# Performance work log

Measured on AMD Instinct MI355X. Metric: run time of the kernel, lower is better.

Reference implementation:

```python
import jax, jax.numpy as jnp
import numpy as np
from functools import partial

TAU = 2.0
BN_EPS = 1e-5
SG_ALPHA = 4.0  # spikingjelly surrogate.Sigmoid default

@jax.custom_vjp
def heaviside(x):
    return (x >= 0.0).astype(x.dtype)

def _heaviside_fwd(x):
    return heaviside(x), x

def _heaviside_bwd(x, g):
    s = jax.nn.sigmoid(SG_ALPHA * x)
    return (g * SG_ALPHA * s * (1.0 - s),)

heaviside.defvjp(_heaviside_fwd, _heaviside_bwd)

def lif(x_seq, v_threshold=1.0):
    # MultiStepLIFNode: tau=2, decay_input=True, v_reset=0 (hard reset), detach_reset
    def step(v, x):
        v = v + (x - v) / TAU
        s = heaviside(v - v_threshold)
        v = v * (1.0 - jax.lax.stop_gradient(s))
        return v, s
    _, s_seq = jax.lax.scan(step, jnp.zeros_like(x_seq[0]), x_seq)
    return s_seq

def conv1x1_bn(x, w, gamma, beta, mean, var, b=None):
    # x: [T,B,C,N]; w: [Cout,Cin]; 1x1 conv == channel matmul; BN in eval mode
    y = jnp.einsum('oc,tbcn->tbon', w, x)
    if b is not None:
        y = y + b[:, None]
    inv = gamma / jnp.sqrt(var + BN_EPS)
    return y * inv[:, None] + (beta - mean * inv)[:, None]

def setup_inputs() -> dict:
    key = jax.random.key(0)
    ks = jax.random.split(key, 24)
    T, B, C, N = 4, 32, 384, 196
    d = {}
    d['x'] = jax.random.normal(ks[0], (T, B, C, N), dtype=jnp.float32)
    d['policy'] = jax.random.uniform(ks[1], (T * B, N, 1), dtype=jnp.float32)
    scale = 1.0 / np.sqrt(C)
    for i, p in enumerate(['q', 'k', 'v', 'proj']):
        base = 2 + i * 5
        d[p + '_w'] = jax.random.normal(ks[base], (C, C), dtype=jnp.float32) * scale
        d[p + '_gamma'] = jnp.ones((C,), jnp.float32)
        d[p + '_beta'] = jnp.zeros((C,), jnp.float32)
        d[p + '_mean'] = jax.random.normal(ks[base + 1], (C,), dtype=jnp.float32) * 0.1
        d[p + '_var'] = jax.random.uniform(ks[base + 2], (C,), dtype=jnp.float32, minval=0.5, maxval=1.5)
    d['proj_b'] = jnp.zeros((C,), jnp.float32)
    return d

def _to_heads(s, H):
    T, B, C, N = s.shape
    # [T,B,C,N] -> [T,B,N,H,D] -> [T,B,H,N,D]
    return s.transpose(0, 1, 3, 2).reshape(T, B, N, H, C // H).transpose(0, 1, 3, 2, 4)

def reference(x, policy, q_w, q_gamma, q_beta, q_mean, q_var,
              k_w, k_gamma, k_beta, k_mean, k_var,
              v_w, v_gamma, v_beta, v_mean, v_var,
              proj_w, proj_gamma, proj_beta, proj_mean, proj_var, proj_b):
    T, B, C, N = x.shape
    H = 12
    attn_scale = 0.25
    q = _to_heads(lif(conv1x1_bn(x, q_w, q_gamma, q_beta, q_mean, q_var)), H)
    k = _to_heads(lif(conv1x1_bn(x, k_w, k_gamma, k_beta, k_mean, k_var)), H)
    v = _to_heads(lif(conv1x1_bn(x, v_w, v_gamma, v_beta, v_mean, v_var)), H)
    attn = jnp.einsum('tbhnd,tbhmd->tbhnm', q, k)
    # attention_policy: attn *= (policy + (1-policy)*eye)
    pol = policy.reshape(T, B, 1, 1, N)
    eye = jnp.eye(N, dtype=attn.dtype)
    attn = attn * (pol + (1.0 - pol) * eye)
    y = jnp.einsum('tbhnm,tbhmd->tbhnd', attn, v) * attn_scale
    y = y.transpose(0, 1, 2, 4, 3).reshape(T, B, C, N)
    y = lif(y, v_threshold=0.5)
    y = conv1x1_bn(y, proj_w, proj_gamma, proj_beta, proj_mean, proj_var, b=proj_b)
    return lif(y)
```

## Files before the change

kernel.cpp:

```cpp
#include <hip/hip_runtime.h>

typedef unsigned int u32;
typedef __bf16 bf16x8 __attribute__((ext_vector_type(8)));
typedef __bf16 bf16x4v __attribute__((ext_vector_type(4)));
typedef _Float16 f16x8 __attribute__((ext_vector_type(8)));
typedef float f32x4 __attribute__((ext_vector_type(4)));

#define Tn 4
#define Bn 32
#define Cn 384
#define Nn 196
#define Hn 12
#define CNn (Cn*Nn)
#define BCNn (Bn*CNn)
#define BHNn (Bn*Hn*Nn)
#define PBITS (Tn*BHNn)
#define TBCNn (Tn*BCNn)
#define NCOLS 6272
#define WSZ 147456

__device__ __forceinline__ void split3(float v, __bf16& h, __bf16& m, __bf16& l) {
  h = (__bf16)v;  float r = v - (float)h;
  m = (__bf16)r;  float r2 = r - (float)m;
  l = (__bf16)r2;
}
__device__ __forceinline__ void split2h(float v, _Float16& h, _Float16& l) {
  h = (_Float16)v;  l = (_Float16)(v - (float)h);
}

__device__ __forceinline__ void gl_lds16(const void* g, void* l) {
  __builtin_amdgcn_global_load_lds(
      (const __attribute__((address_space(1))) unsigned int*)g,
      (__attribute__((address_space(3))) unsigned int*)l, 16, 0, 0);
}

struct WSplitArgs {
  const float* w[4]; const float* g[4]; const float* be[4];
  const float* mu[4]; const float* va[4]; const float* bias;
};
__global__ __launch_bounds__(256) void prep(
    WSplitArgs a, _Float16* __restrict__ wsp16, __bf16* __restrict__ wspb,
    float* __restrict__ shv, const float* __restrict__ x,
    _Float16* __restrict__ xs) {
  __shared__ float tile[49 * 130];
  const int bx = blockIdx.x;
  const int tid = threadIdx.x;
  if (bx < 2304) {
    const int i = bx * 256 + tid;
    const int p = i / WSZ, r = i - p * WSZ;
    const int o = r / Cn, cc = r - o * Cn;
    const float iv = a.g[p][o] / sqrtf(a.va[p][o] + 1e-5f);
    const float wv = a.w[p][r] * iv;
    const int toff = ((o >> 4) * 12 + (cc >> 5)) * 512 +
                     (((cc >> 3) & 3) << 7) + ((o & 15) << 3) + (cc & 7);
    if (p < 3) {
      _Float16 h, l;
      split2h(wv, h, l);
      wsp16[(size_t)(p * 2 + 0) * WSZ + toff] = h;
      wsp16[(size_t)(p * 2 + 1) * WSZ + toff] = l;
    } else {
      __bf16 h, m, l;
      split3(wv, h, m, l);
      wspb[(size_t)0 * WSZ + toff] = h;
      wspb[(size_t)1 * WSZ + toff] = m;
      wspb[(size_t)2 * WSZ + toff] = l;
    }
    if (cc == 0) {
      float sh = a.be[p][o] - a.mu[p][o] * iv;
      if (p == 3) sh += a.bias[o] * iv;
      shv[p * Cn + o] = sh;
    }
    return;
  }
  const int bid2 = bx - 2304;
  const int t = bid2 & 3, b = (bid2 >> 2) & 31, zz = bid2 >> 7;
  const int ct = zz >> 2, nch = zz & 3;
  const int c0 = ct * 128, n0 = nch * 49;
  for (int idx = tid; idx < 49 * 128; idx += 256) {
    const int n = idx % 49, c = idx / 49;
    tile[n * 130 + c] = x[(size_t)t * BCNn + (size_t)b * CNn +
                          (size_t)(c0 + c) * Nn + n0 + n];
  }
  __syncthreads();
  for (int idx = tid; idx < 49 * 64; idx += 256) {
    const int cp = idx & 63, n = idx >> 6;
    const float v0 = tile[n * 130 + cp * 2];
    const float v1 = tile[n * 130 + cp * 2 + 1];
    _Float16 h0, l0, h1, l1;
    split2h(v0, h0, l0);
    split2h(v1, h1, l1);
    const size_t col = (size_t)t * NCOLS + (size_t)b * Nn + n0 + n;
    union { _Float16 f[2]; u32 u; } uh, ul;
    uh.f[0] = h0; uh.f[1] = h1;
    ul.f[0] = l0; ul.f[1] = l1;
    ((u32*)(xs + col * Cn + c0))[cp] = uh.u;
    ((u32*)(xs + (size_t)TBCNn + col * Cn + c0))[cp] = ul.u;
  }
}

__global__ __launch_bounds__(256, 2) void gemm_qkv_lif(
    const _Float16* __restrict__ xs,
    const _Float16* __restrict__ wsp16,
    const float* __restrict__ shv,
    u32* __restrict__ bq, u32* __restrict__ bk, u32* __restrict__ bv)
{
  __shared__ _Float16 Bsw[6][2][64][32];
  const int orig = blockIdx.x;
  const int xcd = orig & 7, i8 = orig >> 3;
  const int wgid = xcd * 110 + (xcd < 2 ? xcd : 2) + i8;
  const int colt = wgid / 9, v = wgid - colt * 9;
  const int col0 = colt * 64;
  const int p = v / 3, mt = v - p * 3;
  const int o0 = mt * 128;
  const int tid = threadIdx.x, lane = tid & 63, wid = tid >> 6;
  const int wm = wid >> 1, wn = wid & 1;
  const int quad = lane >> 4, nl = lane & 15;
  u32* __restrict__ bits = (p == 0) ? bq : (p == 1) ? bk : bv;

  u32 afOff[2][4];
#pragma unroll
  for (int s = 0; s < 2; ++s)
#pragma unroll
    for (int mi = 0; mi < 4; ++mi)
      afOff[s][mi] = (u32)((((p * 2 + s) * WSZ) +
                            (mt * 8 + wm * 4 + mi) * 6144) * 2) +
                     (u32)(lane * 16);
  u32 bOff[2];
#pragma unroll
  for (int i = 0; i < 2; ++i) {
    const int c = i * 256 + wid * 64 + lane;
    const int s = c >> 8, rem = c & 255, row = rem >> 2, kb = rem & 3;
    const int kbs = kb ^ ((row >> 1) & 3);
    bOff[i] = (u32)(((size_t)s * TBCNn + (size_t)(col0 + row) * Cn + kbs * 8) * 2);
  }
  const char* wB = (const char*)wsp16;
  const char* xB = (const char*)xs;
  char* bD0 = (char*)&Bsw[0][0][0][0] + wid * 1024;

#define STAGE_B(g_) do {                                                   \
    const int t_ = ((g_) / 24) * 2 + ((g_) & 1);                           \
    const int kk_ = (((g_) % 24) >> 1);                                    \
    const u32 bk_ = (u32)(kk_ * 64) + (u32)t_ * (u32)(NCOLS * Cn * 2);     \
    char* d_ = bD0 + ((g_) % 6) * 8192;                                    \
    _Pragma("unroll") for (int i_ = 0; i_ < 2; ++i_)                       \
      gl_lds16(xB + bOff[i_] + bk_, d_ + i_ * 4096);                       \
  } while (0)
#define LOAD_AF(DST, g_) do {                                              \
    const u32 ak2_ = (u32)(((g_) % 12) * 1024);                            \
    _Pragma("unroll") for (int s_ = 0; s_ < 2; ++s_)                       \
    _Pragma("unroll") for (int m_ = 0; m_ < 4; ++m_)                       \
      DST[s_][m_] = *(const f16x8*)(wB + afOff[s_][m_] + ak2_);            \
  } while (0)

  f32x4 sh_[4];
#pragma unroll
  for (int mi = 0; mi < 4; ++mi)
    sh_[mi] = *(const f32x4*)&shv[p * Cn + o0 + wm * 64 + mi * 16 + quad * 4];

  f32x4 acc0[4][2], acc1[4][2];
  f32x4 vst[4][2] = {};
  f16x8 afA[2][4], afB[2][4];

  auto epi = [&](f32x4 (&ac)[4][2], int t) {
#pragma unroll
    for (int ni = 0; ni < 2; ++ni) {
      u32 w0 = 0, w1 = 0;
#pragma unroll
      for (int mi = 0; mi < 4; ++mi) {
#pragma unroll
        for (int r = 0; r < 4; ++r) {
          const float y = ac[mi][ni][r] + sh_[mi][r];
          const float vv = vst[mi][ni][r];
          const float nv = vv + (y - vv) * 0.5f;
          const bool sk = nv >= 1.0f;
          vst[mi][ni][r] = sk ? 0.f : nv;
          const u32 b1 = sk ? 1u : 0u;
          const int pos = ((mi & 1) << 4) + (quad << 2) + r;
          if (mi < 2) w0 |= b1 << pos; else w1 |= b1 << pos;
        }
      }
      w0 |= __shfl_xor(w0, 16); w0 |= __shfl_xor(w0, 32);
      w1 |= __shfl_xor(w1, 16); w1 |= __shfl_xor(w1, 32);
      if (quad == 0) {
        const int col = col0 + wn * 32 + ni * 16 + nl;
        const int bb = col / Nn, nn = col - bb * Nn;
        u32* bp = bits + (size_t)t * BHNn +
                  ((size_t)bb * Hn + (mt * 4 + wm * 2)) * Nn + nn;
        bp[0] = w0;
        bp[Nn] = w1;
      }
    }
  };

  auto sub = [&](f16x8 (&afc)[2][4], f16x8 (&afn)[2][4], int g) {
    const int kk = g % 12;
    const int be = (2 * g) % 6, bo = (2 * g + 1) % 6;
    if (g == 23) asm volatile("s_waitcnt vmcnt(8)"  ::: "memory");
    else         asm volatile("s_waitcnt vmcnt(12)" ::: "memory");
    __builtin_amdgcn_s_barrier();
    __builtin_amdgcn_sched_barrier(0);
    if (g < 22) STAGE_B(2 * g + 4);
    if (g < 23) LOAD_AF(afn, g + 1);
    if (g < 22) STAGE_B(2 * g + 5);
    __builtin_amdgcn_sched_barrier(0);
    if (kk == 0) {
#pragma unroll
      for (int mi = 0; mi < 4; ++mi)
#pragma unroll
        for (int ni = 0; ni < 2; ++ni) {
          acc0[mi][ni] = f32x4{0.f, 0.f, 0.f, 0.f};
          acc1[mi][ni] = f32x4{0.f, 0.f, 0.f, 0.f};
        }
    }
    {
      f16x8 bfrE[2][2], bfrO[2][2];
#pragma unroll
      for (int i = 0; i < 2; ++i) {
        const int rb = wn * 32 + i * 16 + nl;
        const int kb2 = (quad ^ ((rb >> 1) & 3)) * 8;
        bfrE[0][i] = *(const f16x8*)&Bsw[be][0][rb][kb2];
        bfrE[1][i] = *(const f16x8*)&Bsw[be][1][rb][kb2];
        bfrO[0][i] = *(const f16x8*)&Bsw[bo][0][rb][kb2];
        bfrO[1][i] = *(const f16x8*)&Bsw[bo][1][rb][kb2];
      }
      __builtin_amdgcn_s_setprio(1);
#pragma unroll
      for (int mi = 0; mi < 4; ++mi)
#pragma unroll
        for (int ni = 0; ni < 2; ++ni) {
          f32x4 c = acc0[mi][ni];
          c = __builtin_amdgcn_mfma_f32_16x16x32_f16(afc[0][mi], bfrE[0][ni], c, 0, 0, 0);
          c = __builtin_amdgcn_mfma_f32_16x16x32_f16(afc[0][mi], bfrE[1][ni], c, 0, 0, 0);
          c = __builtin_amdgcn_mfma_f32_16x16x32_f16(afc[1][mi], bfrE[0][ni], c, 0, 0, 0);
          acc0[mi][ni] = c;
          f32x4 d = acc1[mi][ni];
          d = __builtin_amdgcn_mfma_f32_16x16x32_f16(afc[0][mi], bfrO[0][ni], d, 0, 0, 0);
          d = __builtin_amdgcn_mfma_f32_16x16x32_f16(afc[0][mi], bfrO[1][ni], d, 0, 0, 0);
          d = __builtin_amdgcn_mfma_f32_16x16x32_f16(afc[1][mi], bfrO[0][ni], d, 0, 0, 0);
          acc1[mi][ni] = d;
        }
      __builtin_amdgcn_s_setprio(0);
    }
    if (kk == 11) {
      const int p2 = g / 12;
      epi(acc0, p2 * 2 + 0);
      epi(acc1, p2 * 2 + 1);
    }
  };

  STAGE_B(0); STAGE_B(1); STAGE_B(2);
  LOAD_AF(afA, 0);
  STAGE_B(3);

#pragma unroll 1
  for (int gp = 0; gp < 12; ++gp) {
    sub(afA, afB, 2 * gp);
    sub(afB, afA, 2 * gp + 1);
  }
#undef STAGE_B
#undef LOAD_AF
}

#define USTR 232
#define GSTR 40
__global__ __launch_bounds__(256, 2) void attn_lif(
    const u32* __restrict__ qb, const u32* __restrict__ kb,
    const u32* __restrict__ vb, const float* __restrict__ policy,
    __bf16* __restrict__ sp) {
  __shared__ u32 qs[208], ks[224], vs_[224];
  __shared__ float ps[224];
  __shared__ __bf16 psp[3][224];
  __shared__ __bf16 Ul[3][32][USTR];
  __shared__ __bf16 GT[3][32][GSTR];
  const int bh = blockIdx.x;
  const int bN = bh / Hn;
  const int h = bh - bN * Hn;
  const int tid = threadIdx.x;
  const int lane = tid & 63, wid = tid >> 6;
  const int quad = lane >> 4, nl = lane & 15;
  const int wm1 = wid >> 1, wn1 = wid & 1;
  const __bf16 one = (__bf16)1.0f, zero = (__bf16)0.0f;

  float vst[4][2][4] = {};

  for (int t = 0; t < Tn; ++t) {
    const int tb = t * Bn + bN;
    const int gid = tb * Hn + h;
    if (t) __syncthreads();
    for (int i = tid; i < 224; i += 256) {
      const bool in = i < Nn;
      if (i < 208) qs[i] = in ? qb[(size_t)gid * Nn + i] : 0u;
      ks[i] = in ? kb[(size_t)gid * Nn + i] : 0u;
      vs_[i] = in ? vb[(size_t)gid * Nn + i] : 0u;
      const float p = in ? policy[(size_t)tb * Nn + i] : 0.f;
      ps[i] = p;
      __bf16 hh, mm, ll;
      split3(p, hh, mm, ll);
      psp[0][i] = hh; psp[1][i] = mm; psp[2][i] = ll;
    }
    __syncthreads();

#pragma unroll
    for (int it = 0; it < 7; ++it) {
      const int idx = tid + it * 256;
      const int d = idx & 31, mg = idx >> 5;
      __bf16 u4[3][4];
#pragma unroll
      for (int j = 0; j < 4; ++j) {
        const int m = mg * 4 + j;
        const bool bit = (vs_[m] >> d) & 1u;
#pragma unroll
        for (int s = 0; s < 3; ++s)
          u4[s][j] = bit ? psp[s][m] : zero;
      }
#pragma unroll
      for (int s = 0; s < 3; ++s)
        *(bf16x4v*)&Ul[s][d][mg * 4] = *(bf16x4v*)u4[s];
    }
    __syncthreads();

    f32x4 gacc = {0.f, 0.f, 0.f, 0.f};
    const int crow = wm1 * 16 + nl;
    const int drow = wn1 * 16 + nl;
#pragma unroll
    for (int slab = 0; slab < 7; ++slab) {
      const int m0 = slab * 32 + quad * 8;
      u32 kw[8];
      *(uint4*)&kw[0] = *(const uint4*)&ks[m0];
      *(uint4*)&kw[4] = *(const uint4*)&ks[m0 + 4];
      __bf16 a8[8];
#pragma unroll
      for (int j = 0; j < 8; ++j)
        a8[j] = ((kw[j] >> crow) & 1u) ? one : zero;
      const bf16x8 af = *(const bf16x8*)a8;
#pragma unroll
      for (int s = 0; s < 3; ++s)
        gacc = __builtin_amdgcn_mfma_f32_16x16x32_bf16(
            af, *(const bf16x8*)&Ul[s][drow][slab * 32 + quad * 8], gacc, 0, 0, 0);
    }
#pragma unroll
    for (int r = 0; r < 4; ++r) {
      __bf16 gh, gm, gl;
      split3(gacc[r], gh, gm, gl);
      const int cc = wm1 * 16 + quad * 4 + r;
      GT[0][drow][cc] = gh;
      GT[1][drow][cc] = gm;
      GT[2][drow][cc] = gl;
    }
    __syncthreads();

    bf16x8 bfr2[3][2];
#pragma unroll
    for (int s = 0; s < 3; ++s)
#pragma unroll
      for (int nt = 0; nt < 2; ++nt)
        bfr2[s][nt] = *(const bf16x8*)&GT[s][nt * 16 + nl][quad * 8];

    f32x4 acc2[4][2] = {};
#pragma unroll
    for (int mi = 0; mi < 4; ++mi) {
      const int lt = wid + mi * 4;
      if (lt < 13) {
        const u32 qw = qs[lt * 16 + nl];
        __bf16 a8[8];
#pragma unroll
        for (int j = 0; j < 8; ++j)
          a8[j] = ((qw >> (quad * 8 + j)) & 1u) ? one : zero;
        const bf16x8 af2 = *(const bf16x8*)a8;
#pragma unroll
        for (int nt = 0; nt < 2; ++nt) {
          f32x4 c = acc2[mi][nt];
          c = __builtin_amdgcn_mfma_f32_16x16x32_bf16(af2, bfr2[0][nt], c, 0, 0, 0);
          c = __builtin_amdgcn_mfma_f32_16x16x32_bf16(af2, bfr2[1][nt], c, 0, 0, 0);
          c = __builtin_amdgcn_mfma_f32_16x16x32_bf16(af2, bfr2[2][nt], c, 0, 0, 0);
          acc2[mi][nt] = c;
        }
      }
    }
#pragma unroll
    for (int mi = 0; mi < 4; ++mi) {
      const int lt = wid + mi * 4;
      if (lt >= 13) continue;
#pragma unroll
      for (int r = 0; r < 4; ++r) {
        const int n = lt * 16 + quad * 4 + r;
        if (n >= Nn) continue;
        const float ann = (float)__popc(qs[n] & ks[n]);
        const float wd = ann * (1.0f - ps[n]);
        const u32 vn = vs_[n];
        __bf16* op = sp + (size_t)t * BCNn + ((size_t)bN * Nn + n) * Cn + h * 32;
#pragma unroll
        for (int nt = 0; nt < 2; ++nt) {
          const int d = nt * 16 + nl;
          const float bit = (float)((vn >> d) & 1u);
          const float y = (acc2[mi][nt][r] + wd * bit) * 0.25f;
          const float vv = vst[mi][nt][r];
          const float nv = vv + (y - vv) * 0.5f;
          const bool s = nv >= 0.5f;
          vst[mi][nt][r] = s ? 0.f : nv;
          op[d] = (__bf16)(s ? 1.0f : 0.0f);
        }
      }
    }
  }
}

__global__ __launch_bounds__(256, 3) void gemm_proj_lif(
    const __bf16* __restrict__ sp, const __bf16* __restrict__ wspb,
    const float* __restrict__ shv, float* __restrict__ out)
{
  __shared__ __bf16 Bsw[6][64][32];
  const int orig = blockIdx.x;
  const int xcd = orig & 7, i8 = orig >> 3;
  const int wgid = xcd * 73 + (xcd < 4 ? xcd : 4) + i8;
  const int colt = wgid / 6, ot = wgid - colt * 6;
  const int col0 = colt * 64;
  const int o0 = ot * 64;
  const int tid = threadIdx.x, lane = tid & 63, wid = tid >> 6;
  const int wm = wid >> 1, wn = wid & 1;
  const int quad = lane >> 4, nl = lane & 15;

  u32 afOff[3][2];
#pragma unroll
  for (int s = 0; s < 3; ++s)
#pragma unroll
    for (int mi = 0; mi < 2; ++mi)
      afOff[s][mi] = (u32)(((s * WSZ) + (ot * 4 + wm * 2 + mi) * 6144) * 2) +
                     (u32)(lane * 16);
  u32 bOff;
  {
    const int c = wid * 64 + lane;
    const int row = c >> 2, kb = c & 3;
    const int kbs = kb ^ ((row >> 1) & 3);
    bOff = (u32)(((size_t)(col0 + row) * Cn + kbs * 8) * 2);
  }
  const char* wB = (const char*)wspb;
  const char* sB = (const char*)sp;
  char* bD0 = (char*)&Bsw[0][0][0] + wid * 1024;

#define STAGE_B(g_) do {                                                   \
    const int t_ = ((g_) / 24) * 2 + ((g_) & 1);                           \
    const int kk_ = (((g_) % 24) >> 1);                                    \
    const u32 bk_ = (u32)(kk_ * 64) + (u32)t_ * (u32)(BCNn * 2);           \
    gl_lds16(sB + bOff + bk_, bD0 + ((g_) % 6) * 4096);                    \
  } while (0)
#define LOAD_AF(DST, g_) do {                                              \
    const u32 ak2_ = (u32)(((g_) % 12) * 1024);                            \
    _Pragma("unroll") for (int s_ = 0; s_ < 3; ++s_)                       \
    _Pragma("unroll") for (int m_ = 0; m_ < 2; ++m_)                       \
      DST[s_][m_] = *(const bf16x8*)(wB + afOff[s_][m_] + ak2_);           \
  } while (0)

  f32x4 sh_[2];
#pragma unroll
  for (int mi = 0; mi < 2; ++mi)
    sh_[mi] = *(const f32x4*)&shv[3 * Cn + o0 + wm * 32 + mi * 16 + quad * 4];

  f32x4 acc0[2][2], acc1[2][2];
  f32x4 vst[2][2] = {};
  bf16x8 afA[3][2], afB[3][2];

  auto epi = [&](f32x4 (&ac)[2][2], int t) {
#pragma unroll
    for (int mi = 0; mi < 2; ++mi) {
      const int ob = o0 + wm * 32 + mi * 16 + quad * 4;
#pragma unroll
      for (int ni = 0; ni < 2; ++ni) {
        const int col = col0 + wn * 32 + ni * 16 + nl;
        const int bb = col / Nn, nn = col - bb * Nn;
        float* op = out + (size_t)t * BCNn + (size_t)bb * CNn + nn;
#pragma unroll
        for (int r = 0; r < 4; ++r) {
          const float y = ac[mi][ni][r] + sh_[mi][r];
          const float vv = vst[mi][ni][r];
          const float nv = vv + (y - vv) * 0.5f;
          const bool sk = nv >= 1.0f;
          vst[mi][ni][r] = sk ? 0.f : nv;
          op[(size_t)(ob + r) * Nn] = sk ? 1.0f : 0.0f;
        }
      }
    }
  };

  auto sub = [&](bf16x8 (&afc)[3][2], bf16x8 (&afn)[3][2], int g) {
    const int kk = g % 12;
    const int be = (2 * g) % 6, bo = (2 * g + 1) % 6;
    if (g == 23) asm volatile("s_waitcnt vmcnt(6)" ::: "memory");
    else         asm volatile("s_waitcnt vmcnt(8)" ::: "memory");
    __builtin_amdgcn_s_barrier();
    __builtin_amdgcn_sched_barrier(0);
    if (g < 22) STAGE_B(2 * g + 4);
    if (g < 23) LOAD_AF(afn, g + 1);
    if (g < 22) STAGE_B(2 * g + 5);
    __builtin_amdgcn_sched_barrier(0);
    if (kk == 0) {
#pragma unroll
      for (int mi = 0; mi < 2; ++mi)
#pragma unroll
        for (int ni = 0; ni < 2; ++ni) {
          acc0[mi][ni] = f32x4{0.f, 0.f, 0.f, 0.f};
          acc1[mi][ni] = f32x4{0.f, 0.f, 0.f, 0.f};
        }
    }
    {
      bf16x8 bfrE[2], bfrO[2];
#pragma unroll
      for (int ni = 0; ni < 2; ++ni) {
        const int rb = wn * 32 + ni * 16 + nl;
        const int kb2 = (quad ^ ((rb >> 1) & 3)) * 8;
        bfrE[ni] = *(const bf16x8*)&Bsw[be][rb][kb2];
        bfrO[ni] = *(const bf16x8*)&Bsw[bo][rb][kb2];
      }
      __builtin_amdgcn_s_setprio(1);
#pragma unroll
      for (int mi = 0; mi < 2; ++mi)
#pragma unroll
        for (int ni = 0; ni < 2; ++ni) {
          f32x4 c = acc0[mi][ni];
          c = __builtin_amdgcn_mfma_f32_16x16x32_bf16(afc[0][mi], bfrE[ni], c, 0, 0, 0);
          c = __builtin_amdgcn_mfma_f32_16x16x32_bf16(afc[1][mi], bfrE[ni], c, 0, 0, 0);
          c = __builtin_amdgcn_mfma_f32_16x16x32_bf16(afc[2][mi], bfrE[ni], c, 0, 0, 0);
          acc0[mi][ni] = c;
          f32x4 d = acc1[mi][ni];
          d = __builtin_amdgcn_mfma_f32_16x16x32_bf16(afc[0][mi], bfrO[ni], d, 0, 0, 0);
          d = __builtin_amdgcn_mfma_f32_16x16x32_bf16(afc[1][mi], bfrO[ni], d, 0, 0, 0);
          d = __builtin_amdgcn_mfma_f32_16x16x32_bf16(afc[2][mi], bfrO[ni], d, 0, 0, 0);
          acc1[mi][ni] = d;
        }
      __builtin_amdgcn_s_setprio(0);
    }
    if (kk == 11) {
      const int p2 = g / 12;
      epi(acc0, p2 * 2 + 0);
      epi(acc1, p2 * 2 + 1);
    }
  };

  STAGE_B(0); STAGE_B(1); STAGE_B(2);
  LOAD_AF(afA, 0);
  STAGE_B(3);

#pragma unroll 1
  for (int gp = 0; gp < 12; ++gp) {
    sub(afA, afB, 2 * gp);
    sub(afB, afA, 2 * gp + 1);
  }
#undef STAGE_B
#undef LOAD_AF
}

extern "C" void kernel_launch(void* const* d_in, const int* in_sizes, int n_in,
                              void* d_out, int out_size, void* d_ws, size_t ws_size,
                              hipStream_t stream) {
  const float* x      = (const float*)d_in[0];
  const float* policy = (const float*)d_in[1];
  const float* qw = (const float*)d_in[2];
  const float* qg = (const float*)d_in[3];
  const float* qb_ = (const float*)d_in[4];
  const float* qm = (const float*)d_in[5];
  const float* qv = (const float*)d_in[6];
  const float* kw = (const float*)d_in[7];
  const float* kg = (const float*)d_in[8];
  const float* kbe = (const float*)d_in[9];
  const float* km = (const float*)d_in[10];
  const float* kv = (const float*)d_in[11];
  const float* vw = (const float*)d_in[12];
  const float* vg = (const float*)d_in[13];
  const float* vbe = (const float*)d_in[14];
  const float* vm = (const float*)d_in[15];
  const float* vv = (const float*)d_in[16];
  const float* pw = (const float*)d_in[17];
  const float* pg = (const float*)d_in[18];
  const float* pbe = (const float*)d_in[19];
  const float* pm = (const float*)d_in[20];
  const float* pv = (const float*)d_in[21];
  const float* pbias = (const float*)d_in[22];
  float* out = (float*)d_out;

  char* base = (char*)d_ws;
  _Float16* xs   = (_Float16*)base;
  _Float16* wsp16 = (_Float16*)(base + (size_t)TBCNn * 4);
  __bf16* wspb   = (__bf16*)((char*)wsp16 + (size_t)6 * WSZ * 2);
  float* shv     = (float*)((char*)wspb + (size_t)3 * WSZ * 2);
  u32* bq        = (u32*)((char*)shv + 4 * Cn * 4);
  u32* bk = bq + PBITS;
  u32* bv = bk + PBITS;
  __bf16* sp     = (__bf16*)(bv + PBITS);

  WSplitArgs wa;
  wa.w[0] = qw; wa.g[0] = qg; wa.be[0] = qb_; wa.mu[0] = qm; wa.va[0] = qv;
  wa.w[1] = kw; wa.g[1] = kg; wa.be[1] = kbe; wa.mu[1] = km; wa.va[1] = kv;
  wa.w[2] = vw; wa.g[2] = vg; wa.be[2] = vbe; wa.mu[2] = vm; wa.va[2] = vv;
  wa.w[3] = pw; wa.g[3] = pg; wa.be[3] = pbe; wa.mu[3] = pm; wa.va[3] = pv;
  wa.bias = pbias;
  prep<<<3840, 256, 0, stream>>>(wa, wsp16, wspb, shv, x, xs);

  gemm_qkv_lif<<<882, 256, 0, stream>>>(xs, wsp16, shv, bq, bk, bv);
  attn_lif<<<Bn * Hn, 256, 0, stream>>>(bq, bk, bv, policy, sp);
  gemm_proj_lif<<<588, 256, 0, stream>>>(sp, wspb, shv, out);
}
```

Measured before the change: 268.6 us.

## Process two k-steps per barrier with deeper LDS and register prefetch in QKV GEMM

The QKV GEMM main loop now handles two k-groups per synchronization step instead of one. The shared-memory B ring grows from 6 to 8 stages, and the A-fragment register buffers go from double to quad buffering. This halves the number of s_barrier and waitcnt points and puts more global loads in flight per step, to better hide memory latency. In exchange it uses more LDS and about twice the A-fragment VGPRs, which could cause spills or limit occupancy under launch_bounds(256,2).

```diff
diff --git a/kernel.cpp b/kernel.cpp
--- a/kernel.cpp
+++ b/kernel.cpp
@@ -104,7 +104,7 @@
     const float* __restrict__ shv,
     u32* __restrict__ bq, u32* __restrict__ bk, u32* __restrict__ bv)
 {
-  __shared__ _Float16 Bsw[6][2][64][32];
+  __shared__ _Float16 Bsw[8][2][64][32];
   const int orig = blockIdx.x;
   const int xcd = orig & 7, i8 = orig >> 3;
   const int wgid = xcd * 110 + (xcd < 2 ? xcd : 2) + i8;
@@ -141,7 +141,7 @@
     const int t_ = ((g_) / 24) * 2 + ((g_) & 1);                           \
     const int kk_ = (((g_) % 24) >> 1);                                    \
     const u32 bk_ = (u32)(kk_ * 64) + (u32)t_ * (u32)(NCOLS * Cn * 2);     \
-    char* d_ = bD0 + ((g_) % 6) * 8192;                                    \
+    char* d_ = bD0 + ((g_) % 8) * 8192;                                    \
     _Pragma("unroll") for (int i_ = 0; i_ < 2; ++i_)                       \
       gl_lds16(xB + bOff[i_] + bk_, d_ + i_ * 4096);                       \
   } while (0)
@@ -159,7 +159,7 @@
 
   f32x4 acc0[4][2], acc1[4][2];
   f32x4 vst[4][2] = {};
-  f16x8 afA[2][4], afB[2][4];
+  f16x8 af0[2][4], af1[2][4], af2[2][4], af3[2][4];
 
   auto epi = [&](f32x4 (&ac)[4][2], int t) {
 #pragma unroll
@@ -192,17 +192,9 @@
     }
   };
 
-  auto sub = [&](f16x8 (&afc)[2][4], f16x8 (&afn)[2][4], int g) {
+  auto ggbody = [&](f16x8 (&afc)[2][4], int g) {
     const int kk = g % 12;
-    const int be = (2 * g) % 6, bo = (2 * g + 1) % 6;
-    if (g == 23) asm volatile("s_waitcnt vmcnt(8)"  ::: "memory");
-    else         asm volatile("s_waitcnt vmcnt(12)" ::: "memory");
-    __builtin_amdgcn_s_barrier();
-    __builtin_amdgcn_sched_barrier(0);
-    if (g < 22) STAGE_B(2 * g + 4);
-    if (g < 23) LOAD_AF(afn, g + 1);
-    if (g < 22) STAGE_B(2 * g + 5);
-    __builtin_amdgcn_sched_barrier(0);
+    const int be = (2 * g) % 8, bo = (2 * g + 1) % 8;
     if (kk == 0) {
 #pragma unroll
       for (int mi = 0; mi < 4; ++mi)
@@ -248,14 +240,30 @@
     }
   };
 
-  STAGE_B(0); STAGE_B(1); STAGE_B(2);
-  LOAD_AF(afA, 0);
-  STAGE_B(3);
+  auto sstep = [&](f16x8 (&uA)[2][4], f16x8 (&uB)[2][4],
+                   f16x8 (&lA)[2][4], f16x8 (&lB)[2][4], int S) {
+    asm volatile("s_waitcnt vmcnt(16)" ::: "memory");
+    __builtin_amdgcn_s_barrier();
+    __builtin_amdgcn_sched_barrier(0);
+    if (S < 11) {
+      STAGE_B(4 * S + 4); STAGE_B(4 * S + 5);
+      STAGE_B(4 * S + 6); STAGE_B(4 * S + 7);
+      LOAD_AF(lA, 2 * S + 2);
+      LOAD_AF(lB, 2 * S + 3);
+    }
+    __builtin_amdgcn_sched_barrier(0);
+    ggbody(uA, 2 * S);
+    ggbody(uB, 2 * S + 1);
+  };
+
+  STAGE_B(0); STAGE_B(1); STAGE_B(2); STAGE_B(3);
+  LOAD_AF(af0, 0);
+  LOAD_AF(af1, 1);
 
 #pragma unroll 1
-  for (int gp = 0; gp < 12; ++gp) {
-    sub(afA, afB, 2 * gp);
-    sub(afB, afA, 2 * gp + 1);
+  for (int sp2 = 0; sp2 < 6; ++sp2) {
+    sstep(af0, af1, af2, af3, 2 * sp2);
+    sstep(af2, af3, af0, af1, 2 * sp2 + 1);
   }
 #undef STAGE_B
 #undef LOAD_AF
```

Result: slower. 343.7 us (+28.0%).
